# Kernel tuning notes

Measured on AMD Instinct MI355X. Metric: run time of the kernel, lower is better.

Reference implementation:

```python
import jax, jax.numpy as jnp
import numpy as np

N, K = 10000, 32          # nodes, max neighbors
NUM_ELEM = 100
D_ATOM = 128              # atom embedding size
D_DIR_IN, D_DIR = 10, 64  # node direction expansion -> embedding
D_DIST_IN, D_DIST = 128, 128  # edge distance expansion -> embedding


def setup_inputs() -> dict:
    key = jax.random.key(0)
    ks = jax.random.split(key, 12)
    inp = {
        "atomic_numbers": jax.random.randint(ks[0], (N,), 0, NUM_ELEM),
        "node_direction_expansion": jax.random.normal(ks[1], (N, D_DIR_IN), jnp.float32),
        "edge_distance_expansion": jax.random.normal(ks[2], (N, K, D_DIST_IN), jnp.float32),
        "neighbor_list": jax.random.randint(ks[3], (N, K), 0, N),
        "neighbor_mask": jax.random.randint(ks[4], (N, K), 0, 2).astype(bool),
        # learned params
        "src_atom_emb": jax.random.uniform(ks[5], (NUM_ELEM, D_ATOM), jnp.float32, -0.001, 0.001),
        "tgt_atom_emb": jax.random.uniform(ks[6], (NUM_ELEM, D_ATOM), jnp.float32, -0.001, 0.001),
        "src_dir_W": jax.random.normal(ks[7], (D_DIR_IN, D_DIR), jnp.float32) * 0.1,
        "src_dir_b": jnp.zeros((D_DIR,), jnp.float32),
        "tgt_dir_W": jax.random.normal(ks[8], (D_DIR_IN, D_DIR), jnp.float32) * 0.1,
        "tgt_dir_b": jnp.zeros((D_DIR,), jnp.float32),
        "dist_W": jax.random.normal(ks[9], (D_DIST_IN, D_DIST), jnp.float32) * 0.1,
        "dist_b": jnp.zeros((D_DIST,), jnp.float32),
    }
    return inp


def reference(atomic_numbers, node_direction_expansion, edge_distance_expansion,
              neighbor_list, neighbor_mask,
              src_atom_emb, tgt_atom_emb,
              src_dir_W, src_dir_b, tgt_dir_W, tgt_dir_b, dist_W, dist_b):
    # per-node embeddings
    sa = src_atom_emb[atomic_numbers]                      # [N, D_ATOM]
    ta = tgt_atom_emb[atomic_numbers]                      # [N, D_ATOM]
    sd = jax.nn.silu(node_direction_expansion @ src_dir_W + src_dir_b)  # [N, D_DIR]
    td = jax.nn.silu(node_direction_expansion @ tgt_dir_W + tgt_dir_b)  # [N, D_DIR]

    # map_sender_receiver_feature: sender gathered via neighbor_list, receiver broadcast
    sender_atom = sa[neighbor_list]                        # [N, K, D_ATOM]
    recv_atom = jnp.broadcast_to(ta[:, None, :], (N, K, D_ATOM))
    sender_dir = sd[neighbor_list]                         # [N, K, D_DIR]
    recv_dir = jnp.broadcast_to(td[:, None, :], (N, K, D_DIR))

    edist = jax.nn.silu(edge_distance_expansion @ dist_W + dist_b)  # [N, K, D_DIST]

    edge_features = jnp.concatenate(
        [edist, sender_dir, sender_atom, recv_dir, recv_atom], axis=-1)  # [N, K, 512]

    # masked mean over neighbors
    m = neighbor_mask.astype(edge_features.dtype)          # [N, K]
    count = m.sum(axis=1, keepdims=True) + 1e-5            # [N, 1]
    out = (edge_features * m[:, :, None]).sum(axis=1) / count  # [N, 512]
    return out
```

## Files before the change

### kernel.cpp

```cpp
#include <hip/hip_runtime.h>
#include <hip/hip_bf16.h>

#define NN 10000
#define KK 32
#define DDIRIN 10
#define DDIR 64
#define DD 128

typedef short bf16x8 __attribute__((ext_vector_type(8)));
typedef float f32x4  __attribute__((ext_vector_type(4)));

__device__ __forceinline__ float silu_f(float x) { return x / (1.0f + __expf(-x)); }

__device__ __forceinline__ ushort2 pk_bf16(float a, float b) {
    __hip_bfloat162 h = __float22bfloat162_rn(float2{a, b});
    union { __hip_bfloat162 h; ushort2 u; } v; v.h = h;
    return v.u;
}

__global__ __launch_bounds__(256) void dir_kernel(
    const float* __restrict__ nde,
    const float* __restrict__ sW, const float* __restrict__ sb,
    const float* __restrict__ tW, const float* __restrict__ tb,
    float* __restrict__ sd, float* __restrict__ td)
{
    int gid = blockIdx.x * 256 + threadIdx.x;
    if (gid >= NN * DDIR) return;
    int n = gid >> 6, d = gid & 63;
    float a = sb[d], t = tb[d];
    const float* x = nde + n * DDIRIN;
#pragma unroll
    for (int i = 0; i < DDIRIN; ++i) {
        float xv = x[i];
        a = fmaf(xv, sW[i * DDIR + d], a);
        t = fmaf(xv, tW[i * DDIR + d], t);
    }
    sd[gid] = silu_f(a);
    td[gid] = silu_f(t);
}

__global__ __launch_bounds__(256, 2) void gemm_kernel(
    const float* __restrict__ edist,
    const int*   __restrict__ nmask,
    const float* __restrict__ dW,
    const float* __restrict__ db,
    float* __restrict__ out)
{
    const int tid  = threadIdx.x;
    const int wid  = tid >> 6;
    const int lane = tid & 63;
    const int l15  = lane & 15;
    const int quad = lane >> 4;
    const int n0   = blockIdx.x * 4;

    __shared__ __align__(16) short s_E[128 * 128];
    __shared__ float s_cnt[4];

    bf16x8 bfrag[2][4];
    float  bias[2];
#pragma unroll
    for (int c2 = 0; c2 < 2; ++c2) {
        int ncol = (2 * wid + c2) * 16 + l15;
        bias[c2] = db[ncol];
#pragma unroll
        for (int t = 0; t < 4; ++t) {
            bf16x8 v;
#pragma unroll
            for (int j2 = 0; j2 < 4; ++j2) {
                int k0 = t * 32 + quad * 8 + 2 * j2;
                ushort2 u = pk_bf16(dW[k0 * DD + ncol], dW[(k0 + 1) * DD + ncol]);
                v[2 * j2]     = (short)u.x;
                v[2 * j2 + 1] = (short)u.y;
            }
            bfrag[c2][t] = v;
        }
    }

    {
        const float4* E4 = reinterpret_cast<const float4*>(edist + (size_t)n0 * (KK * DD));
        const int* nm = nmask + n0 * KK;
#pragma unroll
        for (int i = 0; i < 8; ++i) {
            int f0  = 2 * tid + 512 * i;
            int row = f0 >> 5;
            float4 a = E4[f0], b = E4[f0 + 1];
            ushort2 u0 = pk_bf16(a.x, a.y), u1 = pk_bf16(a.z, a.w);
            ushort2 u2 = pk_bf16(b.x, b.y), u3 = pk_bf16(b.z, b.w);
            bf16x8 v;
            v[0] = (short)u0.x; v[1] = (short)u0.y; v[2] = (short)u1.x; v[3] = (short)u1.y;
            v[4] = (short)u2.x; v[5] = (short)u2.y; v[6] = (short)u3.x; v[7] = (short)u3.y;
            bf16x8 z; 
#pragma unroll
            for (int q = 0; q < 8; ++q) z[q] = 0;
            v = (nm[row] != 0) ? v : z;
            int kb = tid & 15;
            int sw = kb ^ (row & 7);
            *reinterpret_cast<bf16x8*>(&s_E[row * 128 + sw * 8]) = v;
        }
        if (tid < 4) {
            int c = 0;
#pragma unroll 8
            for (int k = 0; k < KK; ++k) c += (nm[tid * KK + k] != 0) ? 1 : 0;
            s_cnt[tid] = (float)c;
        }
    }
    __syncthreads();

    f32x4 acc[8][2];
#pragma unroll
    for (int rt = 0; rt < 8; ++rt)
#pragma unroll
        for (int c2 = 0; c2 < 2; ++c2)
#pragma unroll
            for (int g = 0; g < 4; ++g) acc[rt][c2][g] = 0.0f;

#pragma unroll
    for (int rt = 0; rt < 8; ++rt) {
        bf16x8 af[4];
        int r = rt * 16 + l15;
#pragma unroll
        for (int t = 0; t < 4; ++t) {
            int kb = (4 * t + quad) ^ (l15 & 7);
            af[t] = *reinterpret_cast<const bf16x8*>(&s_E[r * 128 + kb * 8]);
        }
#pragma unroll
        for (int t = 0; t < 4; ++t) {
            acc[rt][0] = __builtin_amdgcn_mfma_f32_16x16x32_bf16(af[t], bfrag[0][t], acc[rt][0], 0, 0, 0);
            acc[rt][1] = __builtin_amdgcn_mfma_f32_16x16x32_bf16(af[t], bfrag[1][t], acc[rt][1], 0, 0, 0);
        }
    }

#pragma unroll
    for (int c2 = 0; c2 < 2; ++c2) {
        float sbv = silu_f(bias[c2]);
#pragma unroll
        for (int nd = 0; nd < 4; ++nd) {
            float p = 0.0f;
#pragma unroll
            for (int h = 0; h < 2; ++h) {
                int rt = 2 * nd + h;
#pragma unroll
                for (int g = 0; g < 4; ++g)
                    p += silu_f(acc[rt][c2][g] + bias[c2]);
            }
            p += __shfl_xor(p, 16);
            p += __shfl_xor(p, 32);
            if (quad == nd) {
                float c = s_cnt[nd];
                float val = (p - (32.0f - c) * sbv) / (c + 1e-5f);
                out[(size_t)(n0 + nd) * 512 + (2 * wid + c2) * 16 + l15] = val;
            }
        }
    }
}

template<bool USE_WS>
__global__ __launch_bounds__(256) void seg_kernel(
    const int*   __restrict__ an,
    const float* __restrict__ nde,
    const int*   __restrict__ nl,
    const int*   __restrict__ nmask,
    const float* __restrict__ semb,
    const float* __restrict__ temb,
    const float* __restrict__ sW, const float* __restrict__ sb,
    const float* __restrict__ tW, const float* __restrict__ tb,
    const float* __restrict__ sd_ws,
    const float* __restrict__ td_ws,
    float* __restrict__ out)
{
    const int tid  = threadIdx.x;
    const int wid  = tid >> 6;
    const int lane = tid & 63;
    const int n    = blockIdx.x * 4 + wid;

    __shared__ int s_idx[4][KK];
    __shared__ int s_aidx[4][KK];

    int j = 0; bool act = false;
    if (lane < KK) {
        j   = nl[n * KK + lane];
        act = (nmask[n * KK + lane] != 0);
    }
    unsigned long long bits = __ballot(act);
    int cnt = (int)__popcll(bits);
    if (act) {
        int rank = (int)__popcll(bits & ((1ull << lane) - 1ull));
        s_idx[wid][rank]  = j;
        s_aidx[wid][rank] = an[j];
    }
    __syncthreads();

    const float invv  = 1.0f / ((float)cnt + 1e-5f);
    const float scale = (float)cnt * invv;
    float* outn = out + (size_t)n * 512;

    {
        float s = 0.0f;
        if constexpr (USE_WS) {
#pragma unroll 4
            for (int i = 0; i < cnt; ++i)
                s += sd_ws[s_idx[wid][i] * DDIR + lane];
        } else {
            for (int i = 0; i < cnt; ++i) {
                int jj = s_idx[wid][i];
                float a = sb[lane];
#pragma unroll
                for (int q = 0; q < DDIRIN; ++q)
                    a = fmaf(nde[jj * DDIRIN + q], sW[q * DDIR + lane], a);
                s += silu_f(a);
            }
        }
        outn[128 + lane] = s * invv;
    }

    {
        float s0 = 0.0f, s1 = 0.0f;
#pragma unroll 4
        for (int i = 0; i < cnt; ++i) {
            int a = s_aidx[wid][i];
            s0 += semb[a * DD + lane];
            s1 += semb[a * DD + 64 + lane];
        }
        outn[192 + lane] = s0 * invv;
        outn[256 + lane] = s1 * invv;
    }

    {
        float tdv;
        if constexpr (USE_WS) {
            tdv = td_ws[n * DDIR + lane];
        } else {
            float a = tb[lane];
#pragma unroll
            for (int q = 0; q < DDIRIN; ++q)
                a = fmaf(nde[n * DDIRIN + q], tW[q * DDIR + lane], a);
            tdv = silu_f(a);
        }
        outn[320 + lane] = tdv * scale;
    }

    {
        int ann = an[n];
        outn[384 + lane] = temb[ann * DD + lane] * scale;
        outn[448 + lane] = temb[ann * DD + 64 + lane] * scale;
    }
}

extern "C" void kernel_launch(void* const* d_in, const int* in_sizes, int n_in,
                              void* d_out, int out_size, void* d_ws, size_t ws_size,
                              hipStream_t stream) {
    const int*   an    = (const int*)  d_in[0];
    const float* nde   = (const float*)d_in[1];
    const float* edist = (const float*)d_in[2];
    const int*   nl    = (const int*)  d_in[3];
    const int*   nmask = (const int*)  d_in[4];
    const float* semb  = (const float*)d_in[5];
    const float* temb  = (const float*)d_in[6];
    const float* sW    = (const float*)d_in[7];
    const float* sb    = (const float*)d_in[8];
    const float* tW    = (const float*)d_in[9];
    const float* tb    = (const float*)d_in[10];
    const float* dW    = (const float*)d_in[11];
    const float* db    = (const float*)d_in[12];
    float* out = (float*)d_out;

    gemm_kernel<<<NN / 4, 256, 0, stream>>>(edist, nmask, dW, db, out);

    const size_t need = (size_t)NN * DDIR * sizeof(float) * 2;
    if (ws_size >= need) {
        float* sd = (float*)d_ws;
        float* td = sd + (size_t)NN * DDIR;
        dir_kernel<<<(NN * DDIR + 255) / 256, 256, 0, stream>>>(nde, sW, sb, tW, tb, sd, td);
        seg_kernel<true><<<NN / 4, 256, 0, stream>>>(
            an, nde, nl, nmask, semb, temb, sW, sb, tW, tb, sd, td, out);
    } else {
        seg_kernel<false><<<NN / 4, 256, 0, stream>>>(
            an, nde, nl, nmask, semb, temb, sW, sb, tW, tb, nullptr, nullptr, out);
    }
}
```

Before: 280.7 us.

## Fuse GEMM, direction, and segment kernels into one per-node-block kernel

Merges the distance GEMM kernel, the direction precompute kernel and the segment gather kernel into a single launch. Each block now compacts the neighbor indices, computes the sender direction SiLU on the fly from the 10-wide input with register-held weights, and writes all 512 output columns. This removes two kernel launches and the workspace round trip for the sd/td arrays. In exchange it adds per-neighbor recomputation and extra register pressure in a block already limited to two blocks per CU.

```diff
diff --git a/kernel.cpp b/kernel.cpp
--- a/kernel.cpp
+++ b/kernel.cpp
@@ -18,32 +18,17 @@
     return v.u;
 }
 
-__global__ __launch_bounds__(256) void dir_kernel(
+__global__ __launch_bounds__(256, 2) void gnn_fused_kernel(
+    const int*   __restrict__ an,
     const float* __restrict__ nde,
+    const float* __restrict__ edist,
+    const int*   __restrict__ nl,
+    const int*   __restrict__ nmask,
+    const float* __restrict__ semb,
+    const float* __restrict__ temb,
     const float* __restrict__ sW, const float* __restrict__ sb,
     const float* __restrict__ tW, const float* __restrict__ tb,
-    float* __restrict__ sd, float* __restrict__ td)
-{
-    int gid = blockIdx.x * 256 + threadIdx.x;
-    if (gid >= NN * DDIR) return;
-    int n = gid >> 6, d = gid & 63;
-    float a = sb[d], t = tb[d];
-    const float* x = nde + n * DDIRIN;
-#pragma unroll
-    for (int i = 0; i < DDIRIN; ++i) {
-        float xv = x[i];
-        a = fmaf(xv, sW[i * DDIR + d], a);
-        t = fmaf(xv, tW[i * DDIR + d], t);
-    }
-    sd[gid] = silu_f(a);
-    td[gid] = silu_f(t);
-}
-
-__global__ __launch_bounds__(256, 2) void gemm_kernel(
-    const float* __restrict__ edist,
-    const int*   __restrict__ nmask,
-    const float* __restrict__ dW,
-    const float* __restrict__ db,
+    const float* __restrict__ dW, const float* __restrict__ db,
     float* __restrict__ out)
 {
     const int tid  = threadIdx.x;
@@ -54,7 +39,26 @@
     const int n0   = blockIdx.x * 4;
 
     __shared__ __align__(16) short s_E[128 * 128];
+    __shared__ int   s_idx[4][KK];
+    __shared__ int   s_aidx[4][KK];
     __shared__ float s_cnt[4];
+
+    int cnt;
+    {
+        int j = 0; bool act = false;
+        if (lane < KK) {
+            j   = nl[(n0 + wid) * KK + lane];
+            act = (nmask[(n0 + wid) * KK + lane] != 0);
+        }
+        unsigned long long bits = __ballot(act);
+        cnt = (int)__popcll(bits);
+        if (act) {
+            int rank = (int)__popcll(bits & ((1ull << lane) - 1ull));
+            s_idx[wid][rank]  = j;
+            s_aidx[wid][rank] = an[j];
+        }
+        if (lane == 0) s_cnt[wid] = (float)cnt;
+    }
 
     bf16x8 bfrag[2][4];
     float  bias[2];
@@ -89,19 +93,13 @@
             bf16x8 v;
             v[0] = (short)u0.x; v[1] = (short)u0.y; v[2] = (short)u1.x; v[3] = (short)u1.y;
             v[4] = (short)u2.x; v[5] = (short)u2.y; v[6] = (short)u3.x; v[7] = (short)u3.y;
-            bf16x8 z; 
+            bf16x8 z;
 #pragma unroll
             for (int q = 0; q < 8; ++q) z[q] = 0;
             v = (nm[row] != 0) ? v : z;
             int kb = tid & 15;
             int sw = kb ^ (row & 7);
             *reinterpret_cast<bf16x8*>(&s_E[row * 128 + sw * 8]) = v;
-        }
-        if (tid < 4) {
-            int c = 0;
-#pragma unroll 8
-            for (int k = 0; k < KK; ++k) c += (nm[tid * KK + k] != 0) ? 1 : 0;
-            s_cnt[tid] = (float)c;
         }
     }
     __syncthreads();
@@ -152,97 +150,56 @@
             }
         }
     }
-}
-
-template<bool USE_WS>
-__global__ __launch_bounds__(256) void seg_kernel(
-    const int*   __restrict__ an,
-    const float* __restrict__ nde,
-    const int*   __restrict__ nl,
-    const int*   __restrict__ nmask,
-    const float* __restrict__ semb,
-    const float* __restrict__ temb,
-    const float* __restrict__ sW, const float* __restrict__ sb,
-    const float* __restrict__ tW, const float* __restrict__ tb,
-    const float* __restrict__ sd_ws,
-    const float* __restrict__ td_ws,
-    float* __restrict__ out)
-{
-    const int tid  = threadIdx.x;
-    const int wid  = tid >> 6;
-    const int lane = tid & 63;
-    const int n    = blockIdx.x * 4 + wid;
-
-    __shared__ int s_idx[4][KK];
-    __shared__ int s_aidx[4][KK];
-
-    int j = 0; bool act = false;
-    if (lane < KK) {
-        j   = nl[n * KK + lane];
-        act = (nmask[n * KK + lane] != 0);
-    }
-    unsigned long long bits = __ballot(act);
-    int cnt = (int)__popcll(bits);
-    if (act) {
-        int rank = (int)__popcll(bits & ((1ull << lane) - 1ull));
-        s_idx[wid][rank]  = j;
-        s_aidx[wid][rank] = an[j];
-    }
-    __syncthreads();
-
-    const float invv  = 1.0f / ((float)cnt + 1e-5f);
-    const float scale = (float)cnt * invv;
-    float* outn = out + (size_t)n * 512;
 
     {
-        float s = 0.0f;
-        if constexpr (USE_WS) {
+        const int n = n0 + wid;
+        const float invv  = 1.0f / ((float)cnt + 1e-5f);
+        const float scale = (float)cnt * invv;
+        float* outn = out + (size_t)n * 512;
+
+        {
+            float wreg[DDIRIN];
+#pragma unroll
+            for (int q = 0; q < DDIRIN; ++q) wreg[q] = sW[q * DDIR + lane];
+            float bsv = sb[lane];
+            float s = 0.0f;
+            for (int i = 0; i < cnt; ++i) {
+                const float* x = nde + s_idx[wid][i] * DDIRIN;
+                float a = bsv;
+#pragma unroll
+                for (int q = 0; q < DDIRIN; ++q)
+                    a = fmaf(x[q], wreg[q], a);
+                s += silu_f(a);
+            }
+            outn[128 + lane] = s * invv;
+        }
+
+        {
+            float s0 = 0.0f, s1 = 0.0f;
 #pragma unroll 4
-            for (int i = 0; i < cnt; ++i)
-                s += sd_ws[s_idx[wid][i] * DDIR + lane];
-        } else {
             for (int i = 0; i < cnt; ++i) {
-                int jj = s_idx[wid][i];
-                float a = sb[lane];
-#pragma unroll
-                for (int q = 0; q < DDIRIN; ++q)
-                    a = fmaf(nde[jj * DDIRIN + q], sW[q * DDIR + lane], a);
-                s += silu_f(a);
-            }
-        }
-        outn[128 + lane] = s * invv;
-    }
-
-    {
-        float s0 = 0.0f, s1 = 0.0f;
-#pragma unroll 4
-        for (int i = 0; i < cnt; ++i) {
-            int a = s_aidx[wid][i];
-            s0 += semb[a * DD + lane];
-            s1 += semb[a * DD + 64 + lane];
-        }
-        outn[192 + lane] = s0 * invv;
-        outn[256 + lane] = s1 * invv;
-    }
-
-    {
-        float tdv;
-        if constexpr (USE_WS) {
-            tdv = td_ws[n * DDIR + lane];
-        } else {
+                int a = s_aidx[wid][i];
+                s0 += semb[a * DD + lane];
+                s1 += semb[a * DD + 64 + lane];
+            }
+            outn[192 + lane] = s0 * invv;
+            outn[256 + lane] = s1 * invv;
+        }
+
+        {
             float a = tb[lane];
+            const float* x = nde + n * DDIRIN;
 #pragma unroll
             for (int q = 0; q < DDIRIN; ++q)
-                a = fmaf(nde[n * DDIRIN + q], tW[q * DDIR + lane], a);
-            tdv = silu_f(a);
-        }
-        outn[320 + lane] = tdv * scale;
-    }
-
-    {
-        int ann = an[n];
-        outn[384 + lane] = temb[ann * DD + lane] * scale;
-        outn[448 + lane] = temb[ann * DD + 64 + lane] * scale;
+                a = fmaf(x[q], tW[q * DDIR + lane], a);
+            outn[320 + lane] = silu_f(a) * scale;
+        }
+
+        {
+            int ann = an[n];
+            outn[384 + lane] = temb[ann * DD + lane] * scale;
+            outn[448 + lane] = temb[ann * DD + 64 + lane] * scale;
+        }
     }
 }
 
@@ -264,17 +221,6 @@
     const float* db    = (const float*)d_in[12];
     float* out = (float*)d_out;
 
-    gemm_kernel<<<NN / 4, 256, 0, stream>>>(edist, nmask, dW, db, out);
-
-    const size_t need = (size_t)NN * DDIR * sizeof(float) * 2;
-    if (ws_size >= need) {
-        float* sd = (float*)d_ws;
-        float* td = sd + (size_t)NN * DDIR;
-        dir_kernel<<<(NN * DDIR + 255) / 256, 256, 0, stream>>>(nde, sW, sb, tW, tb, sd, td);
-        seg_kernel<true><<<NN / 4, 256, 0, stream>>>(
-            an, nde, nl, nmask, semb, temb, sW, sb, tW, tb, sd, td, out);
-    } else {
-        seg_kernel<false><<<NN / 4, 256, 0, stream>>>(
-            an, nde, nl, nmask, semb, temb, sW, sb, tW, tb, nullptr, nullptr, out);
-    }
+    gnn_fused_kernel<<<NN / 4, 256, 0, stream>>>(
+        an, nde, edist, nl, nmask, semb, temb, sW, sb, tW, tb, dW, db, out);
 }
```

New measurement: 281.2 us. About the same (+0.2%).
